# Performance work log

Measured on AMD Instinct MI355X. Metric: run time of the kernel, lower is better.

## Reference

```python
import jax, jax.numpy as jnp
import numpy as np

ALPHA = 0.95       # synaptic decay for layers l>0
BETA = 0.9         # membrane decay
THRESHOLD = 1.0
RESET = 0.0        # reset_potential
SIM_T = 100        # simulation_time
SG_SCALE = 100.0   # SuperSpike surrogate-gradient scale (SurrGradSpike)

@jax.custom_vjp
def spike(x):
    # forward: Heaviside step on (mem - threshold)
    return (x > 0).astype(x.dtype)

def _spike_fwd(x):
    return spike(x), x

def _spike_bwd(x, g):
    # SuperSpike surrogate: grad / (scale*|x| + 1)^2
    return (g / (SG_SCALE * jnp.abs(x) + 1.0) ** 2,)

spike.defvjp(_spike_fwd, _spike_bwd)


def setup_inputs() -> dict:
    key = jax.random.key(0)
    k1, k2, k3 = jax.random.split(key, 3)
    B, D, H = 256, 1024, 2048
    inputs = jax.random.normal(k1, (B, D), dtype=jnp.float32)
    w0 = jax.random.normal(k2, (D, H), dtype=jnp.float32) / np.sqrt(D).astype(np.float32)
    w1 = jax.random.normal(k3, (H, H), dtype=jnp.float32) / np.sqrt(H).astype(np.float32)
    return {"inputs": inputs, "w0": w0, "w1": w1}


def _simulate(inputs, w0, w1):
    B = inputs.shape[0]
    H0, H1 = w0.shape[1], w1.shape[1]
    # torch code does inputs.detach().clone() each step -> no grad to inputs
    x = jax.lax.stop_gradient(inputs)

    def step(carry, _):
        s0, m0, s1, m1 = carry
        # layer 0: new_syn = 0*syn + input @ W0
        ns0 = x @ w0
        nm0 = BETA * m0 + ns0
        mthr = nm0 - THRESHOLD          # hidden (non-final) layer spikes
        z = spike(mthr)
        nm0 = jnp.where(mthr > 0, RESET, nm0)   # masked reset after spike
        # layer 1 (final, non-spiking readout): new_syn = alpha*syn + z @ W1
        ns1 = ALPHA * s1 + z @ w1
        nm1 = BETA * m1 + ns1
        return (ns0, nm0, ns1, nm1), (nm0, nm1, z)

    init = (jnp.zeros((B, H0), jnp.float32), jnp.zeros((B, H0), jnp.float32),
            jnp.zeros((B, H1), jnp.float32), jnp.zeros((B, H1), jnp.float32))
    # torch loop records zeros at t==0 and updates for t=1..T-1
    _, (mem0_rec, mem1_rec, spk_rec) = jax.lax.scan(step, init, None, length=SIM_T - 1)
    z0 = jnp.zeros((1, B, H0), jnp.float32)
    z1 = jnp.zeros((1, B, H1), jnp.float32)
    mem0_rec = jnp.concatenate([z0, mem0_rec], axis=0)   # [T, B, H0]
    mem1_rec = jnp.concatenate([z1, mem1_rec], axis=0)   # [T, B, H1]
    spk_rec = jnp.concatenate([z0, spk_rec], axis=0)     # [T, B, H0]
    mem_rec = jnp.stack([mem0_rec, mem1_rec], axis=1)    # [T, L=2, B, H]
    return mem1_rec[-1], mem_rec, spk_rec


def reference(inputs, w0, w1):
    # returns (mem_rec[-1][-1], mem_rec, spk_rec) like the torch module
    return _simulate(inputs, w0, w1)
```

## Files before the change

### kernel.cpp

```cpp
#include <hip/hip_runtime.h>
#include <hip/hip_bf16.h>

#define Bdim 256
#define Ddim 1024
#define Hdim 2048
#define Tdim 100
#define BH (Bdim*Hdim)
#define M3 ((Tdim-1)*Bdim)
#define ZB8 ((size_t)M3*Hdim)

#define OUT_MEM ((size_t)BH)
#define OUT_SPK ((size_t)BH + (size_t)Tdim*2*BH)

typedef __attribute__((ext_vector_type(8))) short short8;
typedef __attribute__((ext_vector_type(4))) float f32x4;
typedef __attribute__((ext_vector_type(4))) int   i32x4;

#define GLD16(g, l) __builtin_amdgcn_global_load_lds( \
    (__attribute__((address_space(1))) void*)(g), \
    (__attribute__((address_space(3))) void*)(l), 16, 0, 0)

static __device__ __forceinline__ unsigned short bf16bits(float f) {
  __hip_bfloat16 h = __float2bfloat16(f);
  return *reinterpret_cast<unsigned short*>(&h);
}

__global__ __launch_bounds__(256) void kcvt_split(const float* __restrict__ X,
                                                  unsigned short* __restrict__ Xhi,
                                                  unsigned short* __restrict__ Xlo) {
  int i = (blockIdx.x*256 + threadIdx.x)*4;
  float4 v = *reinterpret_cast<const float4*>(&X[i]);
  ushort4 ph, pl;
  float f, fh;
  f = v.x; { __hip_bfloat16 h = __float2bfloat16(f); fh = __bfloat162float(h); ph.x = *reinterpret_cast<unsigned short*>(&h); } pl.x = bf16bits(f - fh);
  f = v.y; { __hip_bfloat16 h = __float2bfloat16(f); fh = __bfloat162float(h); ph.y = *reinterpret_cast<unsigned short*>(&h); } pl.y = bf16bits(f - fh);
  f = v.z; { __hip_bfloat16 h = __float2bfloat16(f); fh = __bfloat162float(h); ph.z = *reinterpret_cast<unsigned short*>(&h); } pl.z = bf16bits(f - fh);
  f = v.w; { __hip_bfloat16 h = __float2bfloat16(f); fh = __bfloat162float(h); ph.w = *reinterpret_cast<unsigned short*>(&h); } pl.w = bf16bits(f - fh);
  *reinterpret_cast<ushort4*>(&Xhi[i]) = ph;
  *reinterpret_cast<ushort4*>(&Xlo[i]) = pl;
}

__global__ __launch_bounds__(256) void ktr_split(const float* __restrict__ In,
                                                 unsigned short* __restrict__ OutHi,
                                                 unsigned short* __restrict__ OutLo,
                                                 int R, int C) {
  __shared__ unsigned short thi[32][33];
  __shared__ unsigned short tlo[32][33];
  int bk = blockIdx.x*32, bn = blockIdx.y*32;
  int tx = threadIdx.x & 31, ty = threadIdx.x >> 5;
  for (int r = ty; r < 32; r += 8) {
    float f = In[(size_t)(bk + r)*C + bn + tx];
    __hip_bfloat16 h = __float2bfloat16(f);
    float fh = __bfloat162float(h);
    thi[r][tx] = *reinterpret_cast<unsigned short*>(&h);
    tlo[r][tx] = bf16bits(f - fh);
  }
  __syncthreads();
  for (int r = ty; r < 32; r += 8) {
    OutHi[(size_t)(bn + r)*R + bk + tx] = thi[tx][r];
    OutLo[(size_t)(bn + r)*R + bk + tx] = tlo[tx][r];
  }
}

__global__ __launch_bounds__(256) void kcolmax_part(const float* __restrict__ W1,
                                                    float* __restrict__ pmax) {
  int n = blockIdx.x*256 + threadIdx.x;
  int kc = blockIdx.y;
  float m = 0.f;
  #pragma unroll 8
  for (int k = kc*64; k < kc*64 + 64; ++k)
    m = fmaxf(m, fabsf(W1[(size_t)k*Hdim + n]));
  pmax[(size_t)kc*Hdim + n] = m;
}

__global__ __launch_bounds__(256) void kcolmax_fin(const float* __restrict__ pmax,
                                                   float* __restrict__ scales) {
  int n = blockIdx.x*256 + threadIdx.x;
  float m = 0.f;
  #pragma unroll
  for (int i = 0; i < 32; ++i)
    m = fmaxf(m, pmax[(size_t)i*Hdim + n]);
  scales[n] = m * (1.0f/127.0f);
}

__global__ __launch_bounds__(256) void ktr_i8(const float* __restrict__ In,
                                              const float* __restrict__ scales,
                                              signed char* __restrict__ Out) {
  __shared__ signed char tile[32][33];
  int bk = blockIdx.x*32, bn = blockIdx.y*32;
  int tx = threadIdx.x & 31, ty = threadIdx.x >> 5;
  float rs = 1.0f / scales[bn + tx];
  for (int r = ty; r < 32; r += 8)
    tile[r][tx] = (signed char)(int)rintf(In[(size_t)(bk + r)*Hdim + bn + tx] * rs);
  __syncthreads();
  for (int r = ty; r < 32; r += 8)
    Out[(size_t)(bn + r)*Hdim + bk + tx] = tile[tx][r];
}

#define K1F_NK 32
__global__ __launch_bounds__(256) void k1_fused(const unsigned short* __restrict__ xhi,
                                                const unsigned short* __restrict__ xlo,
                                                const unsigned short* __restrict__ whiT,
                                                const unsigned short* __restrict__ wloT,
                                                float* __restrict__ NS0) {
  __shared__ short Ah[2][64*32], Al[2][64*32];
  __shared__ short Bh[2][64*32], Bl[2][64*32];
  int tid = threadIdx.x;
  int l = tid & 63, w = tid >> 6;
  int wm = w >> 1, wn = w & 1;
  int lr = l & 15, lg = l >> 4;
  size_t gm = (size_t)blockIdx.x * 64;
  size_t gn = (size_t)blockIdx.y * 64;
  int srow = l >> 2;
  int scol = ((l & 3)*8) ^ (((l >> 2) & 6) << 2);
  const unsigned short* gah = &xhi [(gm + w*16 + srow)*1024 + scol];
  const unsigned short* gal = &xlo [(gm + w*16 + srow)*1024 + scol];
  const unsigned short* gbh = &whiT[(gn + w*16 + srow)*1024 + scol];
  const unsigned short* gbl = &wloT[(gn + w*16 + srow)*1024 + scol];
  int rdswz = (lr & 6) << 2;
  f32x4 acc[2][2] = {};
  GLD16(gah, &Ah[0][w*512]); GLD16(gal, &Al[0][w*512]);
  GLD16(gbh, &Bh[0][w*512]); GLD16(gbl, &Bl[0][w*512]);
  __syncthreads();
  #pragma unroll 2
  for (int t = 0; t < K1F_NK; ++t) {
    int cur = t & 1;
    if (t + 1 < K1F_NK) {
      int nxt = cur ^ 1; size_t ko = (size_t)(t + 1)*32;
      GLD16(gah + ko, &Ah[nxt][w*512]); GLD16(gal + ko, &Al[nxt][w*512]);
      GLD16(gbh + ko, &Bh[nxt][w*512]); GLD16(gbl + ko, &Bl[nxt][w*512]);
    }
    short8 ah[2], al[2], bh[2], bl[2];
    #pragma unroll
    for (int mi = 0; mi < 2; ++mi) {
      int ro = (wm*32 + mi*16 + lr)*32 + (lg*8 ^ rdswz);
      ah[mi] = *reinterpret_cast<const short8*>(&Ah[cur][ro]);
      al[mi] = *reinterpret_cast<const short8*>(&Al[cur][ro]);
    }
    #pragma unroll
    for (int ni = 0; ni < 2; ++ni) {
      int ro = (wn*32 + ni*16 + lr)*32 + (lg*8 ^ rdswz);
      bh[ni] = *reinterpret_cast<const short8*>(&Bh[cur][ro]);
      bl[ni] = *reinterpret_cast<const short8*>(&Bl[cur][ro]);
    }
    #pragma unroll
    for (int mi = 0; mi < 2; ++mi)
      #pragma unroll
      for (int ni = 0; ni < 2; ++ni) {
        acc[mi][ni] = __builtin_amdgcn_mfma_f32_16x16x32_bf16(ah[mi], bh[ni], acc[mi][ni], 0, 0, 0);
        acc[mi][ni] = __builtin_amdgcn_mfma_f32_16x16x32_bf16(ah[mi], bl[ni], acc[mi][ni], 0, 0, 0);
        acc[mi][ni] = __builtin_amdgcn_mfma_f32_16x16x32_bf16(al[mi], bh[ni], acc[mi][ni], 0, 0, 0);
      }
    __syncthreads();
  }
  #pragma unroll
  for (int mi = 0; mi < 2; ++mi)
    #pragma unroll
    for (int ni = 0; ni < 2; ++ni)
      #pragma unroll
      for (int q = 0; q < 4; ++q)
        NS0[(gm + wm*32 + mi*16 + lg*4 + q)*Hdim + gn + wn*32 + ni*16 + lr] = acc[mi][ni][q];
}

__global__ __launch_bounds__(256) void k2_sim(const float* __restrict__ NS0,
                                              float* __restrict__ out,
                                              signed char* __restrict__ Zb) {
  size_t i4 = ((size_t)blockIdx.x*256 + threadIdx.x)*4;
  float4 nsv = *reinterpret_cast<const float4*>(&NS0[i4]);
  float ns[4] = {nsv.x, nsv.y, nsv.z, nsv.w};
  float* mem = out + OUT_MEM;
  float* spk = out + OUT_SPK;
  float4 z4 = {0.f, 0.f, 0.f, 0.f};
  *reinterpret_cast<float4*>(&mem[i4]) = z4;
  *reinterpret_cast<float4*>(&mem[BH + i4]) = z4;
  *reinterpret_cast<float4*>(&spk[i4]) = z4;
  float m[4] = {0.f, 0.f, 0.f, 0.f};
  for (int t = 1; t < Tdim; ++t) {
    float4 mo, zf; uchar4 z8;
    #pragma unroll
    for (int j = 0; j < 4; ++j) {
      m[j] = __fadd_rn(__fmul_rn(0.9f, m[j]), ns[j]);
      bool sp = m[j] > 1.0f;
      if (sp) m[j] = 0.f;
      ((float*)&mo)[j] = m[j];
      ((float*)&zf)[j] = sp ? 1.f : 0.f;
      ((unsigned char*)&z8)[j] = sp ? (unsigned char)1 : (unsigned char)0;
    }
    *reinterpret_cast<float4*>(&mem[(size_t)(2*t)*BH + i4]) = mo;
    *reinterpret_cast<float4*>(&spk[(size_t)t*BH + i4]) = zf;
    *reinterpret_cast<uchar4*>(&Zb[(size_t)(t-1)*BH + i4]) = z8;
  }
}

#define NKT3 32

template<int CB>
__global__ __launch_bounds__(256) void k3_gemm(const signed char* __restrict__ A,
                                               const signed char* __restrict__ BT,
                                               const float* __restrict__ scales,
                                               float* __restrict__ mem1,
                                               unsigned short* __restrict__ cbuf) {
  __shared__ signed char As[3][128*64];
  __shared__ signed char Bs[3][128*64];
  int tid = threadIdx.x;
  int l = tid & 63;
  int w = tid >> 6;
  int wm = w >> 1, wn = w & 1;
  int lr = l & 15, lg = l >> 4;
  int rxa = (lr >> 1) & 3;

  int lin = blockIdx.x;
  int wg = (lin & 7)*396 + (lin >> 3);
  int mtile = wg >> 4, ntile = wg & 15;
  size_t gm = (size_t)mtile * 128;
  size_t gn = (size_t)ntile * 128;

  int srow = l >> 2;
  int scol = ((l & 3) ^ ((l >> 3) & 3)) << 4;
  const signed char* gA0 = &A [(gm +      w*16 + srow)*2048 + scol];
  const signed char* gA1 = &A [(gm + 64 + w*16 + srow)*2048 + scol];
  const signed char* gB0 = &BT[(gn +      w*16 + srow)*2048 + scol];
  const signed char* gB1 = &BT[(gn + 64 + w*16 + srow)*2048 + scol];

  #define K3_ST(kt, buf) do { size_t _ko = (size_t)(kt)*64;  \
      GLD16(gA0 + _ko, &As[buf][w*1024]);                     \
      GLD16(gA1 + _ko, &As[buf][4096 + w*1024]);              \
      GLD16(gB0 + _ko, &Bs[buf][w*1024]);                     \
      GLD16(gB1 + _ko, &Bs[buf][4096 + w*1024]); } while (0)

  i32x4 acc[4][4] = {};

  K3_ST(0, 0);
  K3_ST(1, 1);

  int bb = 0;
  for (int kt = 0; kt < NKT3; ++kt) {
    if (kt == NKT3 - 1) asm volatile("s_waitcnt vmcnt(0)" ::: "memory");
    else                asm volatile("s_waitcnt vmcnt(4)" ::: "memory");
    __builtin_amdgcn_s_barrier();
    asm volatile("" ::: "memory");

    int b2 = bb + 2; if (b2 >= 3) b2 -= 3;
    if (kt + 2 < NKT3) K3_ST(kt + 2, b2);

    i32x4 af[4], bf[4];
    #pragma unroll
    for (int mi = 0; mi < 4; ++mi)
      af[mi] = *reinterpret_cast<const i32x4*>(
        &As[bb][(wm*64 + mi*16 + lr)*64 + ((lg ^ rxa)<<4)]);
    #pragma unroll
    for (int ni = 0; ni < 4; ++ni)
      bf[ni] = *reinterpret_cast<const i32x4*>(
        &Bs[bb][(wn*64 + ni*16 + lr)*64 + ((lg ^ rxa)<<4)]);
    #pragma unroll
    for (int mi = 0; mi < 4; ++mi)
      #pragma unroll
      for (int ni = 0; ni < 4; ++ni)
        acc[mi][ni] = __builtin_amdgcn_mfma_i32_16x16x64_i8(af[mi], bf[ni], acc[mi][ni], 0, 0, 0);

    ++bb; if (bb >= 3) bb -= 3;
  }
  #undef K3_ST

  int trow = mtile >> 1;
  int bofs = (mtile & 1) * 128;
  float sc[4];
  #pragma unroll
  for (int ni = 0; ni < 4; ++ni)
    sc[ni] = scales[gn + wn*64 + ni*16 + lr];

  if (CB) {
    unsigned short* cp = cbuf + (size_t)trow*BH + (size_t)bofs*Hdim + gn;
    #pragma unroll
    for (int mi = 0; mi < 4; ++mi)
      #pragma unroll
      for (int ni = 0; ni < 4; ++ni)
        #pragma unroll
        for (int q = 0; q < 4; ++q) {
          int b   = wm*64 + mi*16 + lg*4 + q;
          int col = wn*64 + ni*16 + lr;
          cp[(size_t)b*Hdim + col] = bf16bits((float)acc[mi][ni][q] * sc[ni]);
        }
  } else {
    float* plane = mem1 + (size_t)(2*trow + 3)*BH + (size_t)bofs*Hdim + gn;
    #pragma unroll
    for (int mi = 0; mi < 4; ++mi)
      #pragma unroll
      for (int ni = 0; ni < 4; ++ni)
        #pragma unroll
        for (int q = 0; q < 4; ++q) {
          int b   = wm*64 + mi*16 + lg*4 + q;
          int col = wn*64 + ni*16 + lr;
          plane[(size_t)b*Hdim + col] = (float)acc[mi][ni][q] * sc[ni];
        }
  }
}

__global__ __launch_bounds__(256) void k4_rec(float* __restrict__ out) {
  size_t i4 = ((size_t)blockIdx.x*256 + threadIdx.x)*4;
  float* mem = out + OUT_MEM;
  float s[4] = {0.f,0.f,0.f,0.f}, m[4] = {0.f,0.f,0.f,0.f};
  for (int t = 1; t < Tdim; ++t) {
    float4* p = reinterpret_cast<float4*>(&mem[(size_t)(2*t + 1)*BH + i4]);
    float4 c = *p;
    float4 mo;
    #pragma unroll
    for (int j = 0; j < 4; ++j) {
      s[j] = __fadd_rn(__fmul_rn(0.95f, s[j]), ((float*)&c)[j]);
      m[j] = __fadd_rn(__fmul_rn(0.9f, m[j]), s[j]);
      ((float*)&mo)[j] = m[j];
    }
    *p = mo;
  }
  float4 o = {m[0], m[1], m[2], m[3]};
  *reinterpret_cast<float4*>(&out[i4]) = o;
}

__global__ __launch_bounds__(256) void k4_rec_cb(const unsigned short* __restrict__ C,
                                                 float* __restrict__ out) {
  size_t i4 = ((size_t)blockIdx.x*256 + threadIdx.x)*4;
  float* mem = out + OUT_MEM;
  float s[4] = {0.f,0.f,0.f,0.f}, m[4] = {0.f,0.f,0.f,0.f};
  for (int t = 1; t < Tdim; ++t) {
    ushort4 cv = *reinterpret_cast<const ushort4*>(&C[(size_t)(t-1)*BH + i4]);
    float4 mo;
    #pragma unroll
    for (int j = 0; j < 4; ++j) {
      unsigned int u = ((unsigned short*)&cv)[j];
      float c = __uint_as_float(u << 16);
      s[j] = __fadd_rn(__fmul_rn(0.95f, s[j]), c);
      m[j] = __fadd_rn(__fmul_rn(0.9f, m[j]), s[j]);
      ((float*)&mo)[j] = m[j];
    }
    *reinterpret_cast<float4*>(&mem[(size_t)(2*t + 1)*BH + i4]) = mo;
  }
  float4 o = {m[0], m[1], m[2], m[3]};
  *reinterpret_cast<float4*>(&out[i4]) = o;
}

extern "C" void kernel_launch(void* const* d_in, const int* in_sizes, int n_in,
                              void* d_out, int out_size, void* d_ws, size_t ws_size,
                              hipStream_t stream) {
  const float* X  = (const float*)d_in[0];
  const float* W0 = (const float*)d_in[1];
  const float* W1 = (const float*)d_in[2];
  float* out = (float*)d_out;
  char* ws = (char*)d_ws;

  float*          ns0    = (float*)ws;
  signed char*    w1t8   = (signed char*)(ws + (2ull << 20));
  float*          scales = (float*)(ws + (6ull << 20));
  float*          pmax   = (float*)(ws + (6ull << 20) + (64ull << 10));
  signed char*    zb     = (signed char*)(ws + (10ull << 20));
  unsigned short* cbuf   = (unsigned short*)(ws + (10ull << 20) + ZB8);
  size_t needCb = (10ull << 20) + ZB8 + (size_t)M3*Hdim*2;
  int useCb = (ws_size >= needCb) ? 1 : 0;
  unsigned short* xhi = (unsigned short*)(ws + (10ull << 20));
  unsigned short* xlo = (unsigned short*)(ws + (10ull << 20) + (512<<10));
  unsigned short* whi = (unsigned short*)(ws + (11ull << 20));
  unsigned short* wlo = (unsigned short*)(ws + (15ull << 20));

  kcvt_split  <<<dim3(256),     256, 0, stream>>>(X, xhi, xlo);
  ktr_split   <<<dim3(32, 64),  256, 0, stream>>>(W0, whi, wlo, 1024, 2048);
  kcolmax_part<<<dim3(8, 32),   256, 0, stream>>>(W1, pmax);
  kcolmax_fin <<<dim3(8),       256, 0, stream>>>(pmax, scales);
  ktr_i8      <<<dim3(64, 64),  256, 0, stream>>>(W1, scales, w1t8);
  k1_fused    <<<dim3(4, 32),   256, 0, stream>>>(xhi, xlo, whi, wlo, ns0);
  k2_sim      <<<dim3(BH/1024), 256, 0, stream>>>(ns0, out, zb);
  if (useCb) {
    k3_gemm<1><<<dim3((M3/128)*(Hdim/128)), 256, 0, stream>>>(zb, w1t8, scales, out + OUT_MEM, cbuf);
    k4_rec_cb<<<dim3(BH/1024), 256, 0, stream>>>(cbuf, out);
  } else {
    k3_gemm<0><<<dim3((M3/128)*(Hdim/128)), 256, 0, stream>>>(zb, w1t8, scales, out + OUT_MEM, cbuf);
    k4_rec  <<<dim3(BH/1024), 256, 0, stream>>>(out);
  }
}
```

Measured before the change: 377.5 us.

## Restructure int8 GEMM into single-wave 64x64 workgroups with double-buffered LDS

The k3 int8 GEMM now uses one wavefront per workgroup computing a 64x64 tile instead of four waves sharing a 128x128 tile. Triple buffering becomes double buffering, and the workgroup barrier is replaced by a single-wave lgkmcnt wait before the next prefetch is issued. This is meant to remove barrier synchronisation cost and raise the number of independent workgroups. The trade-off is lower data reuse per tile and more global and L2 traffic, since each A and B row is loaded twice as often overall.

```diff
diff --git a/kernel.cpp b/kernel.cpp
--- a/kernel.cpp
+++ b/kernel.cpp
@@ -195,79 +195,72 @@
 #define NKT3 32
 
 template<int CB>
-__global__ __launch_bounds__(256) void k3_gemm(const signed char* __restrict__ A,
-                                               const signed char* __restrict__ BT,
-                                               const float* __restrict__ scales,
-                                               float* __restrict__ mem1,
-                                               unsigned short* __restrict__ cbuf) {
-  __shared__ signed char As[3][128*64];
-  __shared__ signed char Bs[3][128*64];
-  int tid = threadIdx.x;
-  int l = tid & 63;
-  int w = tid >> 6;
-  int wm = w >> 1, wn = w & 1;
+__global__ __launch_bounds__(64, 2) void k3_gemm(const signed char* __restrict__ A,
+                                                 const signed char* __restrict__ BT,
+                                                 const float* __restrict__ scales,
+                                                 float* __restrict__ mem1,
+                                                 unsigned short* __restrict__ cbuf) {
+  __shared__ signed char As[2][64*64];
+  __shared__ signed char Bs[2][64*64];
+  int l = threadIdx.x;
   int lr = l & 15, lg = l >> 4;
   int rxa = (lr >> 1) & 3;
 
   int lin = blockIdx.x;
-  int wg = (lin & 7)*396 + (lin >> 3);
-  int mtile = wg >> 4, ntile = wg & 15;
-  size_t gm = (size_t)mtile * 128;
-  size_t gn = (size_t)ntile * 128;
+  int wg = (lin & 7)*1584 + (lin >> 3);
+  int mtile = wg >> 5, ntile = wg & 31;
+  size_t gm = (size_t)mtile * 64;
+  size_t gn = (size_t)ntile * 64;
 
   int srow = l >> 2;
   int scol = ((l & 3) ^ ((l >> 3) & 3)) << 4;
-  const signed char* gA0 = &A [(gm +      w*16 + srow)*2048 + scol];
-  const signed char* gA1 = &A [(gm + 64 + w*16 + srow)*2048 + scol];
-  const signed char* gB0 = &BT[(gn +      w*16 + srow)*2048 + scol];
-  const signed char* gB1 = &BT[(gn + 64 + w*16 + srow)*2048 + scol];
-
-  #define K3_ST(kt, buf) do { size_t _ko = (size_t)(kt)*64;  \
-      GLD16(gA0 + _ko, &As[buf][w*1024]);                     \
-      GLD16(gA1 + _ko, &As[buf][4096 + w*1024]);              \
-      GLD16(gB0 + _ko, &Bs[buf][w*1024]);                     \
-      GLD16(gB1 + _ko, &Bs[buf][4096 + w*1024]); } while (0)
+  const signed char* gA = &A [(gm + srow)*2048 + scol];
+  const signed char* gB = &BT[(gn + srow)*2048 + scol];
+
+  #define K3_ST(kt, buf) do { size_t _ko = (size_t)(kt)*64;      \
+      GLD16(gA + _ko,           &As[buf][0]);                     \
+      GLD16(gA + _ko + 16*2048, &As[buf][1024]);                  \
+      GLD16(gA + _ko + 32*2048, &As[buf][2048]);                  \
+      GLD16(gA + _ko + 48*2048, &As[buf][3072]);                  \
+      GLD16(gB + _ko,           &Bs[buf][0]);                     \
+      GLD16(gB + _ko + 16*2048, &Bs[buf][1024]);                  \
+      GLD16(gB + _ko + 32*2048, &Bs[buf][2048]);                  \
+      GLD16(gB + _ko + 48*2048, &Bs[buf][3072]); } while (0)
 
   i32x4 acc[4][4] = {};
 
   K3_ST(0, 0);
   K3_ST(1, 1);
 
-  int bb = 0;
   for (int kt = 0; kt < NKT3; ++kt) {
+    int bb = kt & 1;
     if (kt == NKT3 - 1) asm volatile("s_waitcnt vmcnt(0)" ::: "memory");
-    else                asm volatile("s_waitcnt vmcnt(4)" ::: "memory");
-    __builtin_amdgcn_s_barrier();
-    asm volatile("" ::: "memory");
-
-    int b2 = bb + 2; if (b2 >= 3) b2 -= 3;
-    if (kt + 2 < NKT3) K3_ST(kt + 2, b2);
+    else                asm volatile("s_waitcnt vmcnt(8)" ::: "memory");
 
     i32x4 af[4], bf[4];
     #pragma unroll
     for (int mi = 0; mi < 4; ++mi)
-      af[mi] = *reinterpret_cast<const i32x4*>(
-        &As[bb][(wm*64 + mi*16 + lr)*64 + ((lg ^ rxa)<<4)]);
+      af[mi] = *reinterpret_cast<const i32x4*>(&As[bb][(mi*16 + lr)*64 + ((lg ^ rxa)<<4)]);
     #pragma unroll
     for (int ni = 0; ni < 4; ++ni)
-      bf[ni] = *reinterpret_cast<const i32x4*>(
-        &Bs[bb][(wn*64 + ni*16 + lr)*64 + ((lg ^ rxa)<<4)]);
+      bf[ni] = *reinterpret_cast<const i32x4*>(&Bs[bb][(ni*16 + lr)*64 + ((lg ^ rxa)<<4)]);
     #pragma unroll
     for (int mi = 0; mi < 4; ++mi)
       #pragma unroll
       for (int ni = 0; ni < 4; ++ni)
         acc[mi][ni] = __builtin_amdgcn_mfma_i32_16x16x64_i8(af[mi], bf[ni], acc[mi][ni], 0, 0, 0);
 
-    ++bb; if (bb >= 3) bb -= 3;
+    asm volatile("s_waitcnt lgkmcnt(0)" ::: "memory");
+    if (kt + 2 < NKT3) K3_ST(kt + 2, bb);
   }
   #undef K3_ST
 
-  int trow = mtile >> 1;
-  int bofs = (mtile & 1) * 128;
+  int trow = mtile >> 2;
+  int bofs = (mtile & 3) * 64;
   float sc[4];
   #pragma unroll
   for (int ni = 0; ni < 4; ++ni)
-    sc[ni] = scales[gn + wn*64 + ni*16 + lr];
+    sc[ni] = scales[gn + ni*16 + lr];
 
   if (CB) {
     unsigned short* cp = cbuf + (size_t)trow*BH + (size_t)bofs*Hdim + gn;
@@ -277,8 +270,8 @@
       for (int ni = 0; ni < 4; ++ni)
         #pragma unroll
         for (int q = 0; q < 4; ++q) {
-          int b   = wm*64 + mi*16 + lg*4 + q;
-          int col = wn*64 + ni*16 + lr;
+          int b   = mi*16 + lg*4 + q;
+          int col = ni*16 + lr;
           cp[(size_t)b*Hdim + col] = bf16bits((float)acc[mi][ni][q] * sc[ni]);
         }
   } else {
@@ -289,8 +282,8 @@
       for (int ni = 0; ni < 4; ++ni)
         #pragma unroll
         for (int q = 0; q < 4; ++q) {
-          int b   = wm*64 + mi*16 + lg*4 + q;
-          int col = wn*64 + ni*16 + lr;
+          int b   = mi*16 + lg*4 + q;
+          int col = ni*16 + lr;
           plane[(size_t)b*Hdim + col] = (float)acc[mi][ni][q] * sc[ni];
         }
   }
@@ -368,10 +361,10 @@
   k1_fused    <<<dim3(4, 32),   256, 0, stream>>>(xhi, xlo, whi, wlo, ns0);
   k2_sim      <<<dim3(BH/1024), 256, 0, stream>>>(ns0, out, zb);
   if (useCb) {
-    k3_gemm<1><<<dim3((M3/128)*(Hdim/128)), 256, 0, stream>>>(zb, w1t8, scales, out + OUT_MEM, cbuf);
+    k3_gemm<1><<<dim3((M3/64)*(Hdim/64)), 64, 0, stream>>>(zb, w1t8, scales, out + OUT_MEM, cbuf);
     k4_rec_cb<<<dim3(BH/1024), 256, 0, stream>>>(cbuf, out);
   } else {
-    k3_gemm<0><<<dim3((M3/128)*(Hdim/128)), 256, 0, stream>>>(zb, w1t8, scales, out + OUT_MEM, cbuf);
+    k3_gemm<0><<<dim3((M3/64)*(Hdim/64)), 64, 0, stream>>>(zb, w1t8, scales, out + OUT_MEM, cbuf);
     k4_rec  <<<dim3(BH/1024), 256, 0, stream>>>(out);
   }
 }
```

Result: slower. 434.7 us (+15.2%).
